# Optimization experiments

Hardware: AMD Instinct MI355X
Metric: run time of the kernel (lower is better)

## Reference

```python
import jax, jax.numpy as jnp
import numpy as np

B = 1024
N_NODES = 30
E_PER = 82
IN_F = 128
HID = 256
HEADS = (3, 2, 1)
N_EH = 41


def _lin(k, fi, fo):
    s = 1.0 / np.sqrt(fi)
    kw, kb = jax.random.split(k)
    W = jax.random.uniform(kw, (fi, fo), jnp.float32, -s, s)
    b = jax.random.uniform(kb, (fo,), jnp.float32, -s, s)
    return W, b


def setup_inputs() -> dict:
    key = jax.random.key(0)
    ks = list(jax.random.split(key, 32))
    rng = np.random.default_rng(0)
    # base 30-node graph with E_PER directed edges, no self-loops
    src = rng.integers(0, N_NODES, E_PER)
    dst = (src + rng.integers(1, N_NODES, E_PER)) % N_NODES
    base = np.stack([src, dst])  # [2, E_PER]
    offs = (np.arange(B) * N_NODES)[None, None, :]  # [1,1,B]
    ei = (base[:, :, None] + offs).transpose(0, 2, 1).reshape(2, -1)  # [2, B*E_PER]
    e_h = rng.choice(E_PER, N_EH, replace=False)
    d = {}
    d["x"] = jax.random.normal(ks[0], (B * N_NODES, IN_F), jnp.float32)
    d["edge_index"] = jnp.asarray(ei, dtype=jnp.int32)
    d["e_h_pairs"] = jnp.asarray(base[:, e_h].T, dtype=jnp.int32)  # [N_EH, 2]
    d["Wp"], d["bp"] = _lin(ks[1], IN_F, HID)
    i = 2
    for l, H in enumerate(HEADS):
        d[f"ln_g{l}"] = jnp.ones((HID,), jnp.float32)
        d[f"ln_b{l}"] = jnp.zeros((HID,), jnp.float32)
        d[f"Wl{l}"], d[f"bl{l}"] = _lin(ks[i], HID, H * HID); i += 1
        d[f"Wr{l}"], d[f"br{l}"] = _lin(ks[i], HID, H * HID); i += 1
        d[f"att{l}"] = jax.random.normal(ks[i], (H, HID), jnp.float32) * 0.1; i += 1
        d[f"bias{l}"] = jnp.zeros((HID,), jnp.float32)
    dims = [2 * HID, 256, 128, 128, 1]
    for j in range(4):
        d[f"Wm{j}"], d[f"bm{j}"] = _lin(ks[i], dims[j], dims[j + 1]); i += 1
    return d


def _layer_norm(h, g, b):
    mu = jnp.mean(h, -1, keepdims=True)
    var = jnp.mean((h - mu) ** 2, -1, keepdims=True)
    return (h - mu) * jax.lax.rsqrt(var + 1e-5) * g + b


def _gatv2(h, src, dst, n, Wl, bl, Wr, br, att, bias):
    # PyG GATv2Conv, concat=False (mean over heads), self-loops already in src/dst
    H, C = att.shape
    xl = (h @ Wl + bl).reshape(-1, H, C)  # source transform
    xr = (h @ Wr + br).reshape(-1, H, C)  # target transform
    xj = xl[src]                          # [E,H,C]
    e = jax.nn.leaky_relu(xj + xr[dst], 0.2)
    logits = jnp.einsum('ehc,hc->eh', e, att)  # [E,H]
    m = jax.lax.stop_gradient(jax.ops.segment_max(logits, dst, num_segments=n))
    ex = jnp.exp(logits - m[dst])
    denom = jax.ops.segment_sum(ex, dst, num_segments=n)
    alpha = ex / denom[dst]               # softmax over incoming edges of dst
    out = jax.ops.segment_sum(xj * alpha[..., None], dst, num_segments=n)  # [N,H,C]
    return jnp.mean(out, 1) + bias


def reference(x, edge_index, e_h_pairs, Wp, bp,
              ln_g0, ln_b0, Wl0, bl0, Wr0, br0, att0, bias0,
              ln_g1, ln_b1, Wl1, bl1, Wr1, br1, att1, bias1,
              ln_g2, ln_b2, Wl2, bl2, Wr2, br2, att2, bias2,
              Wm0, bm0, Wm1, bm1, Wm2, bm2, Wm3, bm3):
    n = x.shape[0]
    loops = jnp.arange(n, dtype=edge_index.dtype)
    src = jnp.concatenate([edge_index[0], loops])
    dst = jnp.concatenate([edge_index[1], loops])
    lrelu = lambda v: jax.nn.leaky_relu(v, 0.01)
    h = x @ Wp + bp
    layers = [(ln_g0, ln_b0, Wl0, bl0, Wr0, br0, att0, bias0),
              (ln_g1, ln_b1, Wl1, bl1, Wr1, br1, att1, bias1),
              (ln_g2, ln_b2, Wl2, bl2, Wr2, br2, att2, bias2)]
    for (g, b, Wl, bl, Wr, br, att, bias) in layers:
        hn = _layer_norm(h, g, b)
        hc = _gatv2(hn, src, dst, n, Wl, bl, Wr, br, att, bias)
        h = lrelu(hc) + h  # dropout is identity in eval
    hb = h.reshape(-1, N_NODES, HID)  # [B, 30, 256]
    ef = jnp.concatenate([hb[:, e_h_pairs[:, 0], :], hb[:, e_h_pairs[:, 1], :]], -1)
    o = ef.reshape(-1, 2 * HID)
    o = lrelu(o @ Wm0 + bm0)
    o = lrelu(o @ Wm1 + bm1)
    o = lrelu(o @ Wm2 + bm2)
    o = o @ Wm3 + bm3
    return o.reshape(-1)
```

## Files before the change

kernel.cpp:

```cpp
#include <hip/hip_runtime.h>
#include <hip/hip_bf16.h>
#include <math.h>

#define N_NODES 30
#define E_BASE  82
#define E_TOT   112
#define B_GRAPH 1024
#define HID     256
#define NTOT    (B_GRAPH * N_NODES)
#define MAXIN   32
#define N_EH    41
#define M_MLP   (B_GRAPH * N_EH)

#define META_SRC  0
#define META_DST  E_TOT
#define META_CNT  (2 * E_TOT)
#define META_LIST 256
#define META_INTS 1216

typedef __attribute__((ext_vector_type(8))) short bf16x8;
typedef __attribute__((ext_vector_type(4))) short bf16x4;
typedef __attribute__((ext_vector_type(4))) float f32x4;
#define AS3 __attribute__((address_space(3)))
#define AS1 __attribute__((address_space(1)))

__device__ __forceinline__ void gload_lds16(const void* g, void* l) {
  __builtin_amdgcn_global_load_lds((const AS1 void*)g, (AS3 void*)l, 16, 0, 0);
}

__device__ __forceinline__ float b2f(short s) {
  union { unsigned u; float f; } x;
  x.u = ((unsigned)(unsigned short)s) << 16;
  return x.f;
}

__device__ __forceinline__ short f2bf_bits(float f) {
  union { __hip_bfloat16 h; short s; } u;
  u.h = __float2bfloat16(f);
  return u.s;
}

struct WtJob { const float* in; int K, N, tstart, ooff; };
struct WtArgs { WtJob j[10]; };

__global__ __launch_bounds__(256)
void transpose_weights(WtArgs args, __hip_bfloat16* __restrict__ out,
                       const int* __restrict__ ei, int* __restrict__ meta) {
  int b = blockIdx.x;
  if (b == 976) {
    __shared__ int cnt[N_NODES];
    int tid = threadIdx.x;
    if (tid < N_NODES) cnt[tid] = 0;
    __syncthreads();
    if (tid < E_TOT) {
      int s, d;
      if (tid < E_BASE) { s = ei[tid]; d = ei[B_GRAPH * E_BASE + tid]; }
      else              { s = tid - E_BASE; d = s; }
      meta[META_SRC + tid] = s;
      meta[META_DST + tid] = d;
      int pos = atomicAdd(&cnt[d], 1);
      if (pos < MAXIN) meta[META_LIST + d * MAXIN + pos] = tid;
    }
    __syncthreads();
    if (tid < N_NODES) meta[META_CNT + tid] = cnt[tid];
    return;
  }
  int ji = 0;
  #pragma unroll
  for (int i = 1; i < 10; i++) if (b >= args.j[i].tstart) ji = i;
  WtJob jb = args.j[ji];
  int t = b - jb.tstart;
  int ntn = jb.N >> 5;
  int tk = t / ntn, tn = t - tk * ntn;
  int k0 = tk * 32, n0 = tn * 32;
  __shared__ float s[32][33];
  int tx = threadIdx.x & 31, ty = threadIdx.x >> 5;
  #pragma unroll
  for (int p = 0; p < 4; p++)
    s[ty + p * 8][tx] = jb.in[(size_t)(k0 + ty + p * 8) * jb.N + n0 + tx];
  __syncthreads();
  __hip_bfloat16* o = out + jb.ooff;
  #pragma unroll
  for (int p = 0; p < 4; p++) {
    int n = ty + p * 8;
    o[(size_t)(n0 + n) * jb.K + k0 + tx] = __float2bfloat16(s[tx][n]);
  }
}

#define XP 132
__global__ __launch_bounds__(256)
void gemm_gat(const __hip_bfloat16* __restrict__ A,
              const __hip_bfloat16* __restrict__ Wl,
              const __hip_bfloat16* __restrict__ Wr,
              const float* __restrict__ blv, const float* __restrict__ brv,
              const float* __restrict__ att,
              __hip_bfloat16* __restrict__ xlcat,
              float* __restrict__ logitsG,
              const int* __restrict__ meta, int H)
{
  union GatSmem {
    struct { short a[2][4096]; short b[2][4096]; } st;
    short xlr[128 * XP];
  };
  __shared__ GatSmem sm;
  __shared__ int ssrc[E_TOT], sdst[E_TOT];

  const int tid = threadIdx.x;
  const int lane = tid & 63, wave = tid >> 6;
  const int wx = wave & 1, wy = wave >> 1;
  const int bm = blockIdx.x, bn = blockIdx.y;
  const int mrow = lane & 15, quad = lane >> 4;
  const int hh = bn >> 2, cg = bn & 3;
  const int K = HID;

  if (tid < E_TOT) { ssrc[tid] = meta[META_SRC + tid]; sdst[tid] = meta[META_DST + tid]; }

  const int r0 = tid >> 2, kc0 = (tid & 3) * 8;
  const int Ra = bm * 120 + r0;
  const int Rb = bm * 120 + (r0 + 64 > 119 ? 119 : r0 + 64);
  const __hip_bfloat16* Ag0 = A + (size_t)Ra * K + kc0;
  const __hip_bfloat16* Ag1 = A + (size_t)Rb * K + kc0;
  const int brow = hh * 256 + cg * 64 + r0;
  const __hip_bfloat16* Bg0 = Wl + (size_t)brow * K + kc0;
  const __hip_bfloat16* Bg1 = Wr + (size_t)brow * K + kc0;

  f32x4 acc[4][4];
  #pragma unroll
  for (int i = 0; i < 4; i++)
    #pragma unroll
    for (int j = 0; j < 4; j++)
      acc[i][j] = (f32x4){0.f, 0.f, 0.f, 0.f};

  for (int kt = 0; kt < K; kt += 64) {
    __syncthreads();
    #pragma unroll
    for (int s = 0; s < 2; s++) {
      gload_lds16(Ag0 + kt + s * 32, &sm.st.a[s][tid * 8]);
      gload_lds16(Ag1 + kt + s * 32, &sm.st.a[s][2048 + tid * 8]);
      gload_lds16(Bg0 + kt + s * 32, &sm.st.b[s][tid * 8]);
      gload_lds16(Bg1 + kt + s * 32, &sm.st.b[s][2048 + tid * 8]);
    }
    __syncthreads();

    #pragma unroll
    for (int s = 0; s < 2; s++) {
      bf16x8 af[4], bfr[4];
      #pragma unroll
      for (int i = 0; i < 4; i++) {
        af[i]  = *(const bf16x8*)&sm.st.a[s][(wy * 64 + i * 16 + mrow) * 32 + quad * 8];
        bfr[i] = *(const bf16x8*)&sm.st.b[s][(wx * 64 + i * 16 + mrow) * 32 + quad * 8];
      }
      #pragma unroll
      for (int i = 0; i < 4; i++)
        #pragma unroll
        for (int j = 0; j < 4; j++)
          acc[i][j] = __builtin_amdgcn_mfma_f32_16x16x32_bf16(bfr[j], af[i], acc[i][j], 0, 0, 0);
    }
  }

  __syncthreads();

  const float* bb = wx ? brv : blv;
  #pragma unroll
  for (int i = 0; i < 4; i++) {
    int lrow = wy * 64 + i * 16 + mrow;
    #pragma unroll
    for (int j = 0; j < 4; j++) {
      int c0 = j * 16 + quad * 4;
      float4 bc = *(const float4*)&bb[hh * 256 + cg * 64 + c0];
      short t[4];
      t[0] = f2bf_bits(acc[i][j][0] + bc.x);
      t[1] = f2bf_bits(acc[i][j][1] + bc.y);
      t[2] = f2bf_bits(acc[i][j][2] + bc.z);
      t[3] = f2bf_bits(acc[i][j][3] + bc.w);
      *(bf16x4*)&sm.xlr[lrow * XP + wx * 64 + c0] = *(bf16x4*)t;
    }
  }
  __syncthreads();

  {
    const size_t SROW = (size_t)H * HID;
    #pragma unroll
    for (int p = 0; p < 4; p++) {
      int c = tid + p * 256;
      if (c < 960) {
        int row = c >> 3, part = c & 7;
        bf16x8 v = *(const bf16x8*)&sm.xlr[row * XP + part * 8];
        *(bf16x8*)&((short*)xlcat)[((size_t)bm * 120 + row) * SROW
                                   + hh * HID + cg * 64 + part * 8] = v;
      }
    }
  }

  const int slot = tid >> 3, esub = tid & 7;
  float av[8];
  #pragma unroll
  for (int i = 0; i < 8; i++) av[i] = att[hh * HID + cg * 64 + esub * 8 + i];
  #pragma unroll
  for (int gl = 0; gl < 4; gl++) {
    #pragma unroll
    for (int p = 0; p < 4; p++) {
      int e = p * 32 + slot;
      if (e < E_TOT) {
        int rs = gl * 30 + ssrc[e], rd = gl * 30 + sdst[e];
        bf16x8 xlv = *(const bf16x8*)&sm.xlr[rs * XP + esub * 8];
        bf16x8 xrv = *(const bf16x8*)&sm.xlr[rd * XP + 64 + esub * 8];
        float sum = 0.f;
        #pragma unroll
        for (int i = 0; i < 8; i++) {
          float z = b2f(xlv[i]) + b2f(xrv[i]);
          z = fmaxf(z, 0.2f * z);
          sum = fmaf(z, av[i], sum);
        }
        sum += __shfl_xor(sum, 1);
        sum += __shfl_xor(sum, 2);
        sum += __shfl_xor(sum, 4);
        if (esub == 0)
          atomicAdd(&logitsG[((size_t)(bm * 4 + gl) * H + hh) * E_TOT + e], sum);
      }
    }
  }
}

template<int ACT, int OUTBF>
__global__ __launch_bounds__(256)
void gemm_mfma_f32a(const float* __restrict__ A, const __hip_bfloat16* __restrict__ Bt,
                    const float* __restrict__ bias, void* __restrict__ Cv,
                    int M, int K, int N)
{
  __shared__ __hip_bfloat16 sA[128 * 32];
  __shared__ __hip_bfloat16 sB[128 * 32];
  const int tid = threadIdx.x;
  const int lane = tid & 63;
  const int wave = tid >> 6;
  const int wx = wave & 1, wy = wave >> 1;
  const int bm = blockIdx.x, bn = blockIdx.y;
  const int mrow = lane & 15, quad = lane >> 4;

  const int r0 = tid >> 2, kc0 = (tid & 3) * 8;
  const float* Ag0 = A + (size_t)(bm * 128 + r0) * K + kc0;
  const float* Ag1 = A + (size_t)(bm * 128 + r0 + 64) * K + kc0;
  const __hip_bfloat16* Bg0 = Bt + (size_t)(bn * 128 + r0) * K + kc0;
  const __hip_bfloat16* Bg1 = Bt + (size_t)(bn * 128 + r0 + 64) * K + kc0;

  f32x4 acc[4][4];
  #pragma unroll
  for (int i = 0; i < 4; i++)
    #pragma unroll
    for (int j = 0; j < 4; j++)
      acc[i][j] = (f32x4){0.f, 0.f, 0.f, 0.f};

  for (int kt = 0; kt < K; kt += 32) {
    float4 a00 = *(const float4*)(Ag0 + kt);
    float4 a01 = *(const float4*)(Ag0 + kt + 4);
    float4 a10 = *(const float4*)(Ag1 + kt);
    float4 a11 = *(const float4*)(Ag1 + kt + 4);
    __syncthreads();
    {
      __hip_bfloat16 t[8];
      t[0] = __float2bfloat16(a00.x); t[1] = __float2bfloat16(a00.y);
      t[2] = __float2bfloat16(a00.z); t[3] = __float2bfloat16(a00.w);
      t[4] = __float2bfloat16(a01.x); t[5] = __float2bfloat16(a01.y);
      t[6] = __float2bfloat16(a01.z); t[7] = __float2bfloat16(a01.w);
      *(bf16x8*)&sA[tid * 8] = *(bf16x8*)t;
      t[0] = __float2bfloat16(a10.x); t[1] = __float2bfloat16(a10.y);
      t[2] = __float2bfloat16(a10.z); t[3] = __float2bfloat16(a10.w);
      t[4] = __float2bfloat16(a11.x); t[5] = __float2bfloat16(a11.y);
      t[6] = __float2bfloat16(a11.z); t[7] = __float2bfloat16(a11.w);
      *(bf16x8*)&sA[2048 + tid * 8] = *(bf16x8*)t;
    }
    gload_lds16(Bg0 + kt, &sB[tid * 8]);
    gload_lds16(Bg1 + kt, &sB[2048 + tid * 8]);
    __syncthreads();

    bf16x8 af[4], bfr[4];
    #pragma unroll
    for (int i = 0; i < 4; i++) {
      af[i]  = *(const bf16x8*)&sA[(wy * 64 + i * 16 + mrow) * 32 + quad * 8];
      bfr[i] = *(const bf16x8*)&sB[(wx * 64 + i * 16 + mrow) * 32 + quad * 8];
    }
    #pragma unroll
    for (int i = 0; i < 4; i++)
      #pragma unroll
      for (int j = 0; j < 4; j++)
        acc[i][j] = __builtin_amdgcn_mfma_f32_16x16x32_bf16(af[i], bfr[j], acc[i][j], 0, 0, 0);
  }

  #pragma unroll
  for (int i = 0; i < 4; i++) {
    #pragma unroll
    for (int r = 0; r < 4; r++) {
      size_t row = (size_t)bm * 128 + wy * 64 + i * 16 + quad * 4 + r;
      #pragma unroll
      for (int j = 0; j < 4; j++) {
        int col = bn * 128 + wx * 64 + j * 16 + mrow;
        float v = acc[i][j][r] + bias[col];
        if (ACT) v = v > 0.f ? v : 0.01f * v;
        if (OUTBF) ((__hip_bfloat16*)Cv)[row * N + col] = __float2bfloat16(v);
        else       ((float*)Cv)[row * N + col] = v;
      }
    }
  }
}

__global__ __launch_bounds__(256)
void gemm_mfma_pair(const __hip_bfloat16* __restrict__ hb, const int* __restrict__ pairs,
                    const __hip_bfloat16* __restrict__ Bt, const float* __restrict__ bias,
                    __hip_bfloat16* __restrict__ C, int N)
{
  const int K = 512;
  __shared__ __hip_bfloat16 sA[128 * 32];
  __shared__ __hip_bfloat16 sB[128 * 32];
  const int tid = threadIdx.x;
  const int lane = tid & 63;
  const int wave = tid >> 6;
  const int wx = wave & 1, wy = wave >> 1;
  const int bm = blockIdx.x, bn = blockIdx.y;
  const int mrow = lane & 15, quad = lane >> 4;

  const __hip_bfloat16* pu[2]; const __hip_bfloat16* pv[2]; int sub[2];
  #pragma unroll
  for (int cI = 0; cI < 2; cI++) {
    int c = tid + cI * 256;
    int rc = c >> 2; sub[cI] = (c & 3) * 8;
    int R = bm * 128 + rc;
    int b = R / N_EH, p = R - b * N_EH;
    int u = pairs[p * 2], v = pairs[p * 2 + 1];
    pu[cI] = hb + ((size_t)b * N_NODES + u) * HID;
    pv[cI] = hb + ((size_t)b * N_NODES + v) * HID;
  }

  const int r0 = tid >> 2, kc0 = (tid & 3) * 8;
  const __hip_bfloat16* Bg0 = Bt + (size_t)(bn * 128 + r0) * K + kc0;
  const __hip_bfloat16* Bg1 = Bt + (size_t)(bn * 128 + r0 + 64) * K + kc0;

  f32x4 acc[4][4];
  #pragma unroll
  for (int i = 0; i < 4; i++)
    #pragma unroll
    for (int j = 0; j < 4; j++)
      acc[i][j] = (f32x4){0.f, 0.f, 0.f, 0.f};

  for (int kt = 0; kt < K; kt += 32) {
    __syncthreads();
    #pragma unroll
    for (int cI = 0; cI < 2; cI++) {
      const __hip_bfloat16* src = (kt < 256 ? pu[cI] + kt : pv[cI] + kt - 256) + sub[cI];
      gload_lds16(src, &sA[(size_t)(tid + cI * 256) * 8]);
    }
    gload_lds16(Bg0 + kt, &sB[tid * 8]);
    gload_lds16(Bg1 + kt, &sB[2048 + tid * 8]);
    __syncthreads();

    bf16x8 af[4], bfr[4];
    #pragma unroll
    for (int i = 0; i < 4; i++) {
      af[i]  = *(const bf16x8*)&sA[(wy * 64 + i * 16 + mrow) * 32 + quad * 8];
      bfr[i] = *(const bf16x8*)&sB[(wx * 64 + i * 16 + mrow) * 32 + quad * 8];
    }
    #pragma unroll
    for (int i = 0; i < 4; i++)
      #pragma unroll
      for (int j = 0; j < 4; j++)
        acc[i][j] = __builtin_amdgcn_mfma_f32_16x16x32_bf16(af[i], bfr[j], acc[i][j], 0, 0, 0);
  }

  #pragma unroll
  for (int i = 0; i < 4; i++) {
    #pragma unroll
    for (int r = 0; r < 4; r++) {
      size_t row = (size_t)bm * 128 + wy * 64 + i * 16 + quad * 4 + r;
      #pragma unroll
      for (int j = 0; j < 4; j++) {
        int col = bn * 128 + wx * 64 + j * 16 + mrow;
        float v = acc[i][j][r] + bias[col];
        v = v > 0.f ? v : 0.01f * v;
        C[row * N + col] = __float2bfloat16(v);
      }
    }
  }
}

#define O2P 136
__global__ __launch_bounds__(256)
void mlp_tail(const __hip_bfloat16* __restrict__ o1, const __hip_bfloat16* __restrict__ W1t,
              const float* __restrict__ b1, const __hip_bfloat16* __restrict__ W2t,
              const float* __restrict__ b2, const float* __restrict__ w3,
              const float* __restrict__ b3, float* __restrict__ out)
{
  __shared__ __hip_bfloat16 sA[128 * 32];
  __shared__ __hip_bfloat16 sB[128 * 32];
  __shared__ __hip_bfloat16 sO2[128 * O2P];
  __shared__ float spart[2][128];
  const int tid = threadIdx.x;
  const int lane = tid & 63;
  const int wave = tid >> 6;
  const int wx = wave & 1, wy = wave >> 1;
  const int bm = blockIdx.x;
  const int mrow = lane & 15, quad = lane >> 4;
  const int r0 = tid >> 2, kc0 = (tid & 3) * 8;

  const __hip_bfloat16* Ag0 = o1 + (size_t)(bm * 128 + r0) * 256 + kc0;
  const __hip_bfloat16* Ag1 = o1 + (size_t)(bm * 128 + r0 + 64) * 256 + kc0;
  const __hip_bfloat16* Bg0 = W1t + (size_t)r0 * 256 + kc0;
  const __hip_bfloat16* Bg1 = W1t + (size_t)(r0 + 64) * 256 + kc0;

  f32x4 acc[4][4];
  #pragma unroll
  for (int i = 0; i < 4; i++)
    #pragma unroll
    for (int j = 0; j < 4; j++)
      acc[i][j] = (f32x4){0.f, 0.f, 0.f, 0.f};

  for (int kt = 0; kt < 256; kt += 32) {
    __syncthreads();
    gload_lds16(Ag0 + kt, &sA[tid * 8]);
    gload_lds16(Ag1 + kt, &sA[2048 + tid * 8]);
    gload_lds16(Bg0 + kt, &sB[tid * 8]);
    gload_lds16(Bg1 + kt, &sB[2048 + tid * 8]);
    __syncthreads();

    bf16x8 af[4], bfr[4];
    #pragma unroll
    for (int i = 0; i < 4; i++) {
      af[i]  = *(const bf16x8*)&sA[(wy * 64 + i * 16 + mrow) * 32 + quad * 8];
      bfr[i] = *(const bf16x8*)&sB[(wx * 64 + i * 16 + mrow) * 32 + quad * 8];
    }
    #pragma unroll
    for (int i = 0; i < 4; i++)
      #pragma unroll
      for (int j = 0; j < 4; j++)
        acc[i][j] = __builtin_amdgcn_mfma_f32_16x16x32_bf16(af[i], bfr[j], acc[i][j], 0, 0, 0);
  }

  __syncthreads();
  #pragma unroll
  for (int i = 0; i < 4; i++) {
    #pragma unroll
    for (int r = 0; r < 4; r++) {
      int row = wy * 64 + i * 16 + quad * 4 + r;
      #pragma unroll
      for (int j = 0; j < 4; j++) {
        int col = wx * 64 + j * 16 + mrow;
        float v = acc[i][j][r] + b1[col];
        v = v > 0.f ? v : 0.01f * v;
        sO2[row * O2P + col] = __float2bfloat16(v);
      }
    }
  }

  f32x4 acc2[4][4];
  #pragma unroll
  for (int i = 0; i < 4; i++)
    #pragma unroll
    for (int j = 0; j < 4; j++)
      acc2[i][j] = (f32x4){0.f, 0.f, 0.f, 0.f};

  for (int kt = 0; kt < 128; kt += 32) {
    __syncthreads();
    gload_lds16(W2t + (size_t)r0 * 128 + kt + kc0, &sB[tid * 8]);
    gload_lds16(W2t + (size_t)(r0 + 64) * 128 + kt + kc0, &sB[2048 + tid * 8]);
    __syncthreads();

    bf16x8 af[4], bfr[4];
    #pragma unroll
    for (int i = 0; i < 4; i++) {
      af[i]  = *(const bf16x8*)&sO2[(wy * 64 + i * 16 + mrow) * O2P + kt + quad * 8];
      bfr[i] = *(const bf16x8*)&sB[(wx * 64 + i * 16 + mrow) * 32 + quad * 8];
    }
    #pragma unroll
    for (int i = 0; i < 4; i++)
      #pragma unroll
      for (int j = 0; j < 4; j++)
        acc2[i][j] = __builtin_amdgcn_mfma_f32_16x16x32_bf16(af[i], bfr[j], acc2[i][j], 0, 0, 0);
  }

  float w3v[4], b2v[4];
  #pragma unroll
  for (int j = 0; j < 4; j++) {
    int col = wx * 64 + j * 16 + mrow;
    w3v[j] = w3[col];
    b2v[j] = b2[col];
  }
  #pragma unroll
  for (int i = 0; i < 4; i++) {
    #pragma unroll
    for (int r = 0; r < 4; r++) {
      float s = 0.f;
      #pragma unroll
      for (int j = 0; j < 4; j++) {
        float v = acc2[i][j][r] + b2v[j];
        v = v > 0.f ? v : 0.01f * v;
        s += v * w3v[j];
      }
      #pragma unroll
      for (int off = 8; off; off >>= 1) s += __shfl_xor(s, off);
      if (mrow == 0) {
        int row = wy * 64 + i * 16 + quad * 4 + r;
        spart[wx][row] = s;
      }
    }
  }
  __syncthreads();
  if (tid < 128)
    out[(size_t)bm * 128 + tid] = spart[0][tid] + spart[1][tid] + b3[0];
}

__global__ __launch_bounds__(256)
void layernorm(const float* __restrict__ h, const float* __restrict__ g,
               const float* __restrict__ b, __hip_bfloat16* __restrict__ hn)
{
  const int wv = threadIdx.x >> 6, lane = threadIdx.x & 63;
  const size_t row = (size_t)blockIdx.x * 4 + wv;
  const float* hr = h + row * HID;
  float v[4];
  float sum = 0.f;
  #pragma unroll
  for (int j = 0; j < 4; j++) { v[j] = hr[lane + 64 * j]; sum += v[j]; }
  #pragma unroll
  for (int off = 32; off; off >>= 1) sum += __shfl_xor(sum, off);
  float mu = sum * (1.f / 256.f);
  float vs = 0.f;
  #pragma unroll
  for (int j = 0; j < 4; j++) { float d = v[j] - mu; vs += d * d; }
  #pragma unroll
  for (int off = 32; off; off >>= 1) vs += __shfl_xor(vs, off);
  float rs = rsqrtf(vs * (1.f / 256.f) + 1e-5f);
  __hip_bfloat16* outr = hn + row * HID;
  #pragma unroll
  for (int j = 0; j < 4; j++) {
    int c = lane + 64 * j;
    outr[c] = __float2bfloat16((v[j] - mu) * rs * g[c] + b[c]);
  }
}

template<int DO_LN>
__global__ __launch_bounds__(256, 4)
void gat_agg(const __hip_bfloat16* __restrict__ xcat, const float* __restrict__ logitsG,
             const float* __restrict__ bias, float* __restrict__ h,
             const float* __restrict__ lnG, const float* __restrict__ lnB,
             __hip_bfloat16* __restrict__ hn, const int* __restrict__ meta, int H)
{
  __shared__ __hip_bfloat16 sxl[2][N_NODES * HID];
  __shared__ float salpha[3][E_TOT];
  __shared__ float slog[E_TOT], smax[N_NODES], sden[N_NODES];
  __shared__ int ssrc[E_TOT], sdst[E_TOT], scnt[N_NODES], slist[N_NODES * MAXIN];

  const int tid = threadIdx.x;
  const int g = blockIdx.x;
  const size_t nodebase = (size_t)g * N_NODES;
  const int S = H * HID;
  const int c4 = tid & 63;
  const int ng = tid >> 6;

  if (tid < E_TOT) { ssrc[tid] = meta[META_SRC + tid]; sdst[tid] = meta[META_DST + tid]; }
  if (tid < N_NODES) scnt[tid] = meta[META_CNT + tid];
  for (int i = tid; i < N_NODES * MAXIN; i += 256) slist[i] = meta[META_LIST + i];

  float4 hres[8];
  #pragma unroll
  for (int ki = 0; ki < 8; ki++) {
    int k = ng + ki * 4;
    if (k < N_NODES) hres[ki] = *(const float4*)&h[(nodebase + k) * HID + c4 * 4];
  }

  {
    int i = tid;
    #pragma unroll
    for (int p = 0; p < 4; p++, i += 256) {
      if (i < N_NODES * HID / 8) {
        int node = i >> 5, c = (i & 31) * 8;
        gload_lds16(&xcat[(nodebase + node) * S + 0 * HID + c], &sxl[0][(size_t)i * 8]);
      }
    }
  }

  for (int hh = 0; hh < H; hh++) {
    if (tid < E_TOT) slog[tid] = logitsG[((size_t)g * H + hh) * E_TOT + tid];
    if (tid < N_NODES) sden[tid] = 0.f;
    __syncthreads();
    if (tid < N_NODES) {
      int cnt = scnt[tid];
      const int* lst = &slist[tid * MAXIN];
      float m = -1e30f;
      for (int i = 0; i < cnt; i++) m = fmaxf(m, slog[lst[i]]);
      smax[tid] = m;
    }
    __syncthreads();
    if (tid < E_TOT) {
      float ex = expf(slog[tid] - smax[sdst[tid]]);
      slog[tid] = ex;
      atomicAdd(&sden[sdst[tid]], ex);
    }
    __syncthreads();
    if (tid < E_TOT) salpha[hh][tid] = slog[tid] / sden[sdst[tid]];
  }

  float acc[8][4];
  #pragma unroll
  for (int ki = 0; ki < 8; ki++)
    #pragma unroll
    for (int j = 0; j < 4; j++) acc[ki][j] = 0.f;

  for (int hh = 0; hh < H; hh++) {
    const int buf = hh & 1;
    __syncthreads();
    if (hh + 1 < H) {
      const int nb = buf ^ 1;
      int i = tid;
      #pragma unroll
      for (int p = 0; p < 4; p++, i += 256) {
        if (i < N_NODES * HID / 8) {
          int node = i >> 5, c = (i & 31) * 8;
          gload_lds16(&xcat[(nodebase + node) * S + (hh + 1) * HID + c], &sxl[nb][(size_t)i * 8]);
        }
      }
    }
    #pragma unroll
    for (int ki = 0; ki < 8; ki++) {
      int k = ng + ki * 4;
      if (k < N_NODES) {
        int cnt = scnt[k];
        const int* lst = &slist[k * MAXIN];
        for (int i = 0; i < cnt; i++) {
          int e = lst[i];
          float al = salpha[hh][e];
          bf16x4 v = *(const bf16x4*)&sxl[buf][ssrc[e] * HID + c4 * 4];
          acc[ki][0] += al * b2f(v[0]);
          acc[ki][1] += al * b2f(v[1]);
          acc[ki][2] += al * b2f(v[2]);
          acc[ki][3] += al * b2f(v[3]);
        }
      }
    }
  }

  const float invH = 1.f / (float)H;
  const float4 bs = *(const float4*)&bias[c4 * 4];
  float4 gv, bv;
  if (DO_LN) {
    gv = *(const float4*)&lnG[c4 * 4];
    bv = *(const float4*)&lnB[c4 * 4];
  }
  #pragma unroll
  for (int ki = 0; ki < 8; ki++) {
    int k = ng + ki * 4;
    if (k < N_NODES) {
      float o0 = acc[ki][0] * invH + bs.x; o0 = o0 > 0.f ? o0 : 0.01f * o0; o0 += hres[ki].x;
      float o1 = acc[ki][1] * invH + bs.y; o1 = o1 > 0.f ? o1 : 0.01f * o1; o1 += hres[ki].y;
      float o2 = acc[ki][2] * invH + bs.z; o2 = o2 > 0.f ? o2 : 0.01f * o2; o2 += hres[ki].z;
      float o3 = acc[ki][3] * invH + bs.w; o3 = o3 > 0.f ? o3 : 0.01f * o3; o3 += hres[ki].w;
      float4 o4 = {o0, o1, o2, o3};
      *(float4*)&h[(nodebase + k) * HID + c4 * 4] = o4;
      if (DO_LN) {
        float sum = o0 + o1 + o2 + o3;
        #pragma unroll
        for (int off = 32; off; off >>= 1) sum += __shfl_xor(sum, off);
        float mu = sum * (1.f / 256.f);
        float d0 = o0 - mu, d1 = o1 - mu, d2 = o2 - mu, d3 = o3 - mu;
        float vs = d0 * d0 + d1 * d1 + d2 * d2 + d3 * d3;
        #pragma unroll
        for (int off = 32; off; off >>= 1) vs += __shfl_xor(vs, off);
        float rs = rsqrtf(vs * (1.f / 256.f) + 1e-5f);
        __hip_bfloat16 t[4];
        t[0] = __float2bfloat16(d0 * rs * gv.x + bv.x);
        t[1] = __float2bfloat16(d1 * rs * gv.y + bv.y);
        t[2] = __float2bfloat16(d2 * rs * gv.z + bv.z);
        t[3] = __float2bfloat16(d3 * rs * gv.w + bv.w);
        *(bf16x4*)&hn[(nodebase + k) * HID + c4 * 4] = *(bf16x4*)t;
      } else {
        short t[4];
        t[0] = f2bf_bits(o0); t[1] = f2bf_bits(o1);
        t[2] = f2bf_bits(o2); t[3] = f2bf_bits(o3);
        *(bf16x4*)&hn[(nodebase + k) * HID + c4 * 4] = *(bf16x4*)t;
      }
    }
  }
}

extern "C" void kernel_launch(void* const* d_in, const int* in_sizes, int n_in,
                              void* d_out, int out_size, void* d_ws, size_t ws_size,
                              hipStream_t stream) {
  const float* x     = (const float*)d_in[0];
  const int*   ei    = (const int*)d_in[1];
  const int*   pairs = (const int*)d_in[2];
  const float* bp    = (const float*)d_in[4];
  const float *lng[3], *lnb[3], *bl[3], *br[3], *att[3], *bias[3];
  const float *WlF[3], *WrF[3];
  for (int l = 0; l < 3; l++) {
    int base = 5 + l * 8;
    lng[l]  = (const float*)d_in[base + 0];
    lnb[l]  = (const float*)d_in[base + 1];
    WlF[l]  = (const float*)d_in[base + 2];
    bl[l]   = (const float*)d_in[base + 3];
    WrF[l]  = (const float*)d_in[base + 4];
    br[l]   = (const float*)d_in[base + 5];
    att[l]  = (const float*)d_in[base + 6];
    bias[l] = (const float*)d_in[base + 7];
  }
  const float* WmF[4] = {(const float*)d_in[29], (const float*)d_in[31],
                         (const float*)d_in[33], (const float*)d_in[35]};
  const float* bm[4] = {(const float*)d_in[30], (const float*)d_in[32],
                        (const float*)d_in[34], (const float*)d_in[36]};

  float* ws  = (float*)d_ws;
  float* h   = ws;
  __hip_bfloat16* hnb = (__hip_bfloat16*)(ws + 7864320);
  __hip_bfloat16* xlcat = (__hip_bfloat16*)(ws + 11796480);
  float* logits0 = ws + 30000000;
  float* logits1 = logits0 + 344064;
  float* logits2 = logits1 + 229376;
  __hip_bfloat16* wbuf = (__hip_bfloat16*)(ws + 35733504);
  int*   meta = (int*)(ws + 36233216);
  __hip_bfloat16* o1b = (__hip_bfloat16*)xlcat;
  float* out = (float*)d_out;

  hipMemsetAsync(logits0, 0, (344064 + 229376 + 114688) * sizeof(float), stream);

  const int oWp = 0, oWl0 = 32768, oWr0 = 229376, oWl1 = 425984, oWr1 = 557056;
  const int oWl2 = 688128, oWr2 = 753664, oWm0 = 819200, oWm1 = 950272, oWm2 = 983040;

  WtArgs wa;
  wa.j[0] = {(const float*)d_in[3], 128, 256,   0, oWp };
  wa.j[1] = {WlF[0],              256, 768,  32, oWl0};
  wa.j[2] = {WrF[0],              256, 768, 224, oWr0};
  wa.j[3] = {WlF[1],              256, 512, 416, oWl1};
  wa.j[4] = {WrF[1],              256, 512, 544, oWr1};
  wa.j[5] = {WlF[2],              256, 256, 672, oWl2};
  wa.j[6] = {WrF[2],              256, 256, 736, oWr2};
  wa.j[7] = {WmF[0],              512, 256, 800, oWm0};
  wa.j[8] = {WmF[1],              256, 128, 928, oWm1};
  wa.j[9] = {WmF[2],              128, 128, 960, oWm2};
  transpose_weights<<<977, 256, 0, stream>>>(wa, wbuf, ei, meta);

  gemm_mfma_f32a<0, 0><<<dim3(NTOT / 128, 2), 256, 0, stream>>>(x, wbuf + oWp, bp, h,
                                                                NTOT, 128, 256);

  layernorm<<<NTOT / 4, 256, 0, stream>>>(h, lng[0], lnb[0], hnb);

  const int Hs[3] = {3, 2, 1};
  const int oWl[3] = {oWl0, oWl1, oWl2};
  const int oWr[3] = {oWr0, oWr1, oWr2};
  float* logitsL[3] = {logits0, logits1, logits2};
  for (int l = 0; l < 3; l++) {
    int H = Hs[l];
    gemm_gat<<<dim3(NTOT / 120, H * 4), 256, 0, stream>>>(
        hnb, wbuf + oWl[l], wbuf + oWr[l], bl[l], br[l], att[l],
        xlcat, logitsL[l], meta, H);
    if (l < 2)
      gat_agg<1><<<B_GRAPH, 256, 0, stream>>>(xlcat, logitsL[l], bias[l], h,
                                              lng[l + 1], lnb[l + 1], hnb, meta, H);
    else
      gat_agg<0><<<B_GRAPH, 256, 0, stream>>>(xlcat, logitsL[l], bias[l], h,
                                              nullptr, nullptr, hnb, meta, H);
  }

  gemm_mfma_pair<<<dim3(M_MLP / 128, 2), 256, 0, stream>>>(hnb, pairs, wbuf + oWm0, bm[0], o1b, 256);
  mlp_tail<<<M_MLP / 128, 256, 0, stream>>>(o1b, wbuf + oWm1, bm[1], wbuf + oWm2, bm[2],
                                            WmF[3], bm[3], out);
}
```

Baseline: 431.6 us.

## Fold logits memset into prep kernel, batch softmax across heads, vectorize layernorm

Zeroes the logits buffers inside the weight-transpose kernel with extra blocks instead of a separate memset. It packs each edge's source node into the per-node edge list so aggregation no longer needs a separate src lookup. All heads' softmax statistics are now computed together, which cuts the number of barriers in the aggregation kernel. The layernorm kernel switches to float4 loads and bf16x4 stores, and the xlcat global store in the GAT GEMM moves after the logit computation.

```diff
diff --git a/kernel.cpp b/kernel.cpp
--- a/kernel.cpp
+++ b/kernel.cpp
@@ -45,8 +45,14 @@
 
 __global__ __launch_bounds__(256)
 void transpose_weights(WtArgs args, __hip_bfloat16* __restrict__ out,
-                       const int* __restrict__ ei, int* __restrict__ meta) {
+                       const int* __restrict__ ei, int* __restrict__ meta,
+                       float* __restrict__ logitsZ) {
   int b = blockIdx.x;
+  if (b >= 977) {
+    int base = (b - 977) * 4096 + threadIdx.x * 4;
+    *(float4*)&logitsZ[base] = (float4){0.f, 0.f, 0.f, 0.f};
+    return;
+  }
   if (b == 976) {
     __shared__ int cnt[N_NODES];
     int tid = threadIdx.x;
@@ -59,7 +65,7 @@
       meta[META_SRC + tid] = s;
       meta[META_DST + tid] = d;
       int pos = atomicAdd(&cnt[d], 1);
-      if (pos < MAXIN) meta[META_LIST + d * MAXIN + pos] = tid;
+      if (pos < MAXIN) meta[META_LIST + d * MAXIN + pos] = (tid << 8) | s;
     }
     __syncthreads();
     if (tid < N_NODES) meta[META_CNT + tid] = cnt[tid];
@@ -177,20 +183,6 @@
     }
   }
   __syncthreads();
-
-  {
-    const size_t SROW = (size_t)H * HID;
-    #pragma unroll
-    for (int p = 0; p < 4; p++) {
-      int c = tid + p * 256;
-      if (c < 960) {
-        int row = c >> 3, part = c & 7;
-        bf16x8 v = *(const bf16x8*)&sm.xlr[row * XP + part * 8];
-        *(bf16x8*)&((short*)xlcat)[((size_t)bm * 120 + row) * SROW
-                                   + hh * HID + cg * 64 + part * 8] = v;
-      }
-    }
-  }
 
   const int slot = tid >> 3, esub = tid & 7;
   float av[8];
@@ -220,6 +212,20 @@
       }
     }
   }
+
+  {
+    const size_t SROW = (size_t)H * HID;
+    #pragma unroll
+    for (int p = 0; p < 4; p++) {
+      int c = tid + p * 256;
+      if (c < 960) {
+        int row = c >> 3, part = c & 7;
+        bf16x8 v = *(const bf16x8*)&sm.xlr[row * XP + part * 8];
+        *(bf16x8*)&((short*)xlcat)[((size_t)bm * 120 + row) * SROW
+                                   + hh * HID + cg * 64 + part * 8] = v;
+      }
+    }
+  }
 }
 
 template<int ACT, int OUTBF>
@@ -513,25 +519,24 @@
   const int wv = threadIdx.x >> 6, lane = threadIdx.x & 63;
   const size_t row = (size_t)blockIdx.x * 4 + wv;
   const float* hr = h + row * HID;
-  float v[4];
-  float sum = 0.f;
-  #pragma unroll
-  for (int j = 0; j < 4; j++) { v[j] = hr[lane + 64 * j]; sum += v[j]; }
+  float4 v = *(const float4*)&hr[lane * 4];
+  float sum = v.x + v.y + v.z + v.w;
   #pragma unroll
   for (int off = 32; off; off >>= 1) sum += __shfl_xor(sum, off);
   float mu = sum * (1.f / 256.f);
-  float vs = 0.f;
-  #pragma unroll
-  for (int j = 0; j < 4; j++) { float d = v[j] - mu; vs += d * d; }
+  float d0 = v.x - mu, d1 = v.y - mu, d2 = v.z - mu, d3 = v.w - mu;
+  float vs = d0 * d0 + d1 * d1 + d2 * d2 + d3 * d3;
   #pragma unroll
   for (int off = 32; off; off >>= 1) vs += __shfl_xor(vs, off);
   float rs = rsqrtf(vs * (1.f / 256.f) + 1e-5f);
-  __hip_bfloat16* outr = hn + row * HID;
-  #pragma unroll
-  for (int j = 0; j < 4; j++) {
-    int c = lane + 64 * j;
-    outr[c] = __float2bfloat16((v[j] - mu) * rs * g[c] + b[c]);
-  }
+  float4 gv = *(const float4*)&g[lane * 4];
+  float4 bv = *(const float4*)&b[lane * 4];
+  short t[4];
+  t[0] = f2bf_bits(d0 * rs * gv.x + bv.x);
+  t[1] = f2bf_bits(d1 * rs * gv.y + bv.y);
+  t[2] = f2bf_bits(d2 * rs * gv.z + bv.z);
+  t[3] = f2bf_bits(d3 * rs * gv.w + bv.w);
+  *(bf16x4*)&hn[row * HID + lane * 4] = *(bf16x4*)t;
 }
 
 template<int DO_LN>
@@ -542,9 +547,9 @@
              __hip_bfloat16* __restrict__ hn, const int* __restrict__ meta, int H)
 {
   __shared__ __hip_bfloat16 sxl[2][N_NODES * HID];
-  __shared__ float salpha[3][E_TOT];
-  __shared__ float slog[E_TOT], smax[N_NODES], sden[N_NODES];
-  __shared__ int ssrc[E_TOT], sdst[E_TOT], scnt[N_NODES], slist[N_NODES * MAXIN];
+  __shared__ float slogA[3 * 128], salphaA[3 * 128];
+  __shared__ float smaxA[3 * 32], sdenA[3 * 32];
+  __shared__ int sdst[E_TOT], scnt[N_NODES], slist[N_NODES * MAXIN];
 
   const int tid = threadIdx.x;
   const int g = blockIdx.x;
@@ -553,7 +558,7 @@
   const int c4 = tid & 63;
   const int ng = tid >> 6;
 
-  if (tid < E_TOT) { ssrc[tid] = meta[META_SRC + tid]; sdst[tid] = meta[META_DST + tid]; }
+  if (tid < E_TOT) sdst[tid] = meta[META_DST + tid];
   if (tid < N_NODES) scnt[tid] = meta[META_CNT + tid];
   for (int i = tid; i < N_NODES * MAXIN; i += 256) slist[i] = meta[META_LIST + i];
 
@@ -575,25 +580,35 @@
     }
   }
 
-  for (int hh = 0; hh < H; hh++) {
-    if (tid < E_TOT) slog[tid] = logitsG[((size_t)g * H + hh) * E_TOT + tid];
-    if (tid < N_NODES) sden[tid] = 0.f;
-    __syncthreads();
-    if (tid < N_NODES) {
-      int cnt = scnt[tid];
-      const int* lst = &slist[tid * MAXIN];
+  for (int i = tid; i < H * 128; i += 256) {
+    int hh = i >> 7, e = i & 127;
+    if (e < E_TOT) slogA[i] = logitsG[((size_t)g * H + hh) * E_TOT + e];
+  }
+  if (tid < H * 32) sdenA[tid] = 0.f;
+  __syncthreads();
+  {
+    int hh = tid >> 5, node = tid & 31;
+    if (hh < H && node < N_NODES) {
+      int cnt = scnt[node];
+      const int* lst = &slist[node * MAXIN];
       float m = -1e30f;
-      for (int i = 0; i < cnt; i++) m = fmaxf(m, slog[lst[i]]);
-      smax[tid] = m;
-    }
-    __syncthreads();
-    if (tid < E_TOT) {
-      float ex = expf(slog[tid] - smax[sdst[tid]]);
-      slog[tid] = ex;
-      atomicAdd(&sden[sdst[tid]], ex);
-    }
-    __syncthreads();
-    if (tid < E_TOT) salpha[hh][tid] = slog[tid] / sden[sdst[tid]];
+      for (int i = 0; i < cnt; i++) m = fmaxf(m, slogA[(hh << 7) + (lst[i] >> 8)]);
+      smaxA[tid] = m;
+    }
+  }
+  __syncthreads();
+  for (int i = tid; i < H * 128; i += 256) {
+    int hh = i >> 7, e = i & 127;
+    if (e < E_TOT) {
+      float ex = expf(slogA[i] - smaxA[(hh << 5) + sdst[e]]);
+      slogA[i] = ex;
+      atomicAdd(&sdenA[(hh << 5) + sdst[e]], ex);
+    }
+  }
+  __syncthreads();
+  for (int i = tid; i < H * 128; i += 256) {
+    int hh = i >> 7, e = i & 127;
+    if (e < E_TOT) salphaA[i] = slogA[i] / sdenA[(hh << 5) + sdst[e]];
   }
 
   float acc[8][4];
@@ -623,9 +638,9 @@
         int cnt = scnt[k];
         const int* lst = &slist[k * MAXIN];
         for (int i = 0; i < cnt; i++) {
-          int e = lst[i];
-          float al = salpha[hh][e];
-          bf16x4 v = *(const bf16x4*)&sxl[buf][ssrc[e] * HID + c4 * 4];
+          int pk = lst[i];
+          float al = salphaA[(hh << 7) + (pk >> 8)];
+          bf16x4 v = *(const bf16x4*)&sxl[buf][(pk & 255) * HID + c4 * 4];
           acc[ki][0] += al * b2f(v[0]);
           acc[ki][1] += al * b2f(v[1]);
           acc[ki][2] += al * b2f(v[2]);
@@ -715,8 +730,6 @@
   __hip_bfloat16* o1b = (__hip_bfloat16*)xlcat;
   float* out = (float*)d_out;
 
-  hipMemsetAsync(logits0, 0, (344064 + 229376 + 114688) * sizeof(float), stream);
-
   const int oWp = 0, oWl0 = 32768, oWr0 = 229376, oWl1 = 425984, oWr1 = 557056;
   const int oWl2 = 688128, oWr2 = 753664, oWm0 = 819200, oWm1 = 950272, oWm2 = 983040;
 
@@ -731,7 +744,7 @@
   wa.j[7] = {WmF[0],              512, 256, 800, oWm0};
   wa.j[8] = {WmF[1],              256, 128, 928, oWm1};
   wa.j[9] = {WmF[2],              128, 128, 960, oWm2};
-  transpose_weights<<<977, 256, 0, stream>>>(wa, wbuf, ei, meta);
+  transpose_weights<<<1145, 256, 0, stream>>>(wa, wbuf, ei, meta, logits0);
 
   gemm_mfma_f32a<0, 0><<<dim3(NTOT / 128, 2), 256, 0, stream>>>(x, wbuf + oWp, bp, h,
                                                                 NTOT, 128, 256);
```

Measured after the change: 425.5 us. About the same (-1.4%).
